# Performance work log

Measured on AMD Instinct MI355X. Metric: run time of the kernel, lower is better.

## Reference

```python
import jax, jax.numpy as jnp
import numpy as np

N = 1024    # num_points
HID = 1024  # Hamiltonian MLP hidden width


def setup_inputs() -> dict:
    key = jax.random.key(0)
    ks = jax.random.split(key, 6)
    def w(k, shape, fan_in):
        return jax.random.normal(k, shape, dtype=jnp.float32) / np.float32(np.sqrt(fan_in))
    return {
        "x": jax.random.normal(ks[0], (N,), dtype=jnp.float32),
        "q": jax.random.normal(ks[1], (N,), dtype=jnp.float32),
        "p": jax.random.normal(ks[2], (N,), dtype=jnp.float32),
        "W1": w(ks[3], (3 * N, HID), 3 * N),
        "b1": jnp.zeros((HID,), dtype=jnp.float32),
        "W2": w(ks[4], (HID, HID), HID),
        "b2": jnp.zeros((HID,), dtype=jnp.float32),
        "W3": w(ks[5], (HID, 1), HID),
        "b3": jnp.zeros((1,), dtype=jnp.float32),
    }


def _hamiltonian(z, W1, b1, W2, b2, W3, b3):
    # H: R^{3N} -> scalar (matches self.H(cat([x,q,p])).sum())
    h = jnp.tanh(z @ W1 + b1)
    h = jnp.tanh(h @ W2 + b2)
    return jnp.sum(h @ W3 + b3)


def reference(x, q, p, W1, b1, W2, b2, W3, b3):
    n = x.shape[0]

    def grads_qp(x_):
        # (dH/dq, dH/dp) as a function of x, with q,p closed over
        f = lambda q_, p_: _hamiltonian(jnp.concatenate([x_, q_, p_]), W1, b1, W2, b2, W3, b3)
        return jax.grad(f, argnums=(0, 1))(q, p)  # each [n]

    # Diagonal of cross-Hessian blocks via forward-over-reverse, batched over
    # all n basis directions at once (replaces the per-index autograd loop).
    eye = jnp.eye(n, dtype=x.dtype)

    def diag_entry(e_i, i):
        _, (dgq, dgp) = jax.jvp(grads_qp, (x,), (e_i,))
        return dgq[i], dgp[i]  # d2H/(dx_i dq_i), d2H/(dx_i dp_i)

    dH_dq_dx, dH_dp_dx = jax.vmap(diag_entry)(eye, jnp.arange(n))  # each [n]
    return dH_dp_dx, -dH_dq_dx
```

## Files before the change

kernel.cpp:

```cpp
#include <hip/hip_runtime.h>
#include <math.h>

typedef unsigned short u16;
typedef __bf16 bf16x8 __attribute__((ext_vector_type(8)));
typedef float f32x4 __attribute__((ext_vector_type(4)));

__device__ inline u16 bf16_rn(float x) {
    unsigned u = __float_as_uint(x);
    return (u16)((u + 0x7FFFu + ((u >> 16) & 1u)) >> 16);
}
__device__ inline void split2(float x, u16& h, u16& l) {
    h = bf16_rn(x);
    float hf = __uint_as_float(((unsigned)h) << 16);
    l = bf16_rn(x - hf);
}
__device__ inline uint2 pack4(u16 a, u16 b, u16 c, u16 d) {
    uint2 r;
    r.x = (unsigned)a | ((unsigned)b << 16);
    r.y = (unsigned)c | ((unsigned)d << 16);
    return r;
}
__device__ inline f32x4 mfma16(bf16x8 a, bf16x8 b, f32x4 c) {
    return __builtin_amdgcn_mfma_f32_16x16x32_bf16(a, b, c, 0, 0, 0);
}

__global__ __launch_bounds__(256) void k_init(const float* __restrict__ x,
                                              const float* __restrict__ q,
                                              const float* __restrict__ p,
                                              float* __restrict__ Z,
                                              float* __restrict__ out,
                                              float* __restrict__ uv) {
    int j = blockIdx.x * 256 + threadIdx.x;
    if (j < 2048) { out[j] = 0.f; uv[j] = 0.f; }
    Z[j] = (j < 1024) ? x[j] : (j < 2048 ? q[j - 1024] : p[j - 2048]);
}

__global__ __launch_bounds__(256) void k_u_partial(const float* __restrict__ W1,
                                                   const float* __restrict__ Z,
                                                   float* __restrict__ Uacc) {
    int k = blockIdx.x * 256 + threadIdx.x;
    int j0 = blockIdx.y * 64;
    __shared__ float zs[64];
    if (threadIdx.x < 64) zs[threadIdx.x] = Z[j0 + threadIdx.x];
    __syncthreads();
    float acc = 0.f;
#pragma unroll 8
    for (int j = 0; j < 64; ++j) acc += zs[j] * W1[(j0 + j) * 1024 + k];
    atomicAdd(&Uacc[k], acc);
}

__global__ __launch_bounds__(256) void k_h1(const float* __restrict__ Uacc,
                                            const float* __restrict__ b1,
                                            float* __restrict__ H1, float* __restrict__ D1) {
    int k = blockIdx.x * 256 + threadIdx.x;
    float h = tanhf(Uacc[k] + b1[k]);
    H1[k] = h;
    D1[k] = 1.f - h * h;
}

__global__ __launch_bounds__(256) void k_v_partial(const float* __restrict__ W2,
                                                   const float* __restrict__ H1,
                                                   float* __restrict__ Vacc) {
    int m = blockIdx.x * 256 + threadIdx.x;
    int k0 = blockIdx.y * 64;
    __shared__ float hs[64];
    if (threadIdx.x < 64) hs[threadIdx.x] = H1[k0 + threadIdx.x];
    __syncthreads();
    float acc = 0.f;
#pragma unroll 8
    for (int k = 0; k < 64; ++k) acc += hs[k] * W2[(k0 + k) * 1024 + m];
    atomicAdd(&Vacc[m], acc);
}

__global__ __launch_bounds__(256) void k_h2(const float* __restrict__ Vacc,
                                            const float* __restrict__ b2,
                                            const float* __restrict__ W3,
                                            float* __restrict__ Svec, float* __restrict__ Cvec) {
    int m = blockIdx.x * 256 + threadIdx.x;
    float h = tanhf(Vacc[m] + b2[m]);
    float d2 = 1.f - h * h;
    float w3 = W3[m];
    Svec[m] = d2 * w3;
    Cvec[m] = -2.f * h * d2 * w3;
}

__global__ __launch_bounds__(256) void k_g(const float* __restrict__ W2,
                                           const float* __restrict__ Svec,
                                           const float* __restrict__ H1,
                                           const float* __restrict__ D1,
                                           float* __restrict__ Avec) {
    int k = blockIdx.x;
    int t = threadIdx.x;
    float acc = 0.f;
#pragma unroll
    for (int m = t; m < 1024; m += 256) acc += W2[k * 1024 + m] * Svec[m];
    for (int o = 32; o; o >>= 1) acc += __shfl_down(acc, o);
    __shared__ float red[4];
    int lane = t & 63, w = t >> 6;
    if (lane == 0) red[w] = acc;
    __syncthreads();
    if (t == 0) Avec[k] = -2.f * H1[k] * D1[k] * (red[0] + red[1] + red[2] + red[3]);
}

__global__ __launch_bounds__(256) void k_prep_a(const float* __restrict__ W1,
                                                u16* __restrict__ Ah, u16* __restrict__ Al) {
    int idx = (blockIdx.x * 256 + threadIdx.x) * 4;
    float4 v = *(const float4*)(W1 + idx);
    u16 h0, l0, h1, l1, h2, l2, h3, l3;
    split2(v.x, h0, l0); split2(v.y, h1, l1); split2(v.z, h2, l2); split2(v.w, h3, l3);
    *(uint2*)&Ah[idx] = pack4(h0, h1, h2, h3);
    *(uint2*)&Al[idx] = pack4(l0, l1, l2, l3);
}

__global__ __launch_bounds__(256) void k_prep_w2(const float* __restrict__ W2,
                                                 const float* __restrict__ D1,
                                                 u16* __restrict__ W2h, u16* __restrict__ W2l,
                                                 u16* __restrict__ WTh, u16* __restrict__ WTl) {
    __shared__ float T[64][65];
    int k0 = blockIdx.y * 64, m0 = blockIdx.x * 64;
    int t = threadIdx.x;
    int rr = t >> 4, cc = (t & 15) * 4;
#pragma unroll
    for (int j = 0; j < 4; ++j) {
        int r = rr + j * 16;
        float4 v = *(const float4*)(W2 + (k0 + r) * 1024 + m0 + cc);
        T[r][cc + 0] = v.x; T[r][cc + 1] = v.y; T[r][cc + 2] = v.z; T[r][cc + 3] = v.w;
        u16 h0, l0, h1, l1, h2, l2, h3, l3;
        split2(v.x, h0, l0); split2(v.y, h1, l1); split2(v.z, h2, l2); split2(v.w, h3, l3);
        *(uint2*)&W2h[(k0 + r) * 1024 + m0 + cc] = pack4(h0, h1, h2, h3);
        *(uint2*)&W2l[(k0 + r) * 1024 + m0 + cc] = pack4(l0, l1, l2, l3);
    }
    __syncthreads();
#pragma unroll
    for (int j = 0; j < 4; ++j) {
        int mrow = rr + j * 16;
        float f0 = T[cc + 0][mrow] * D1[k0 + cc + 0];
        float f1 = T[cc + 1][mrow] * D1[k0 + cc + 1];
        float f2 = T[cc + 2][mrow] * D1[k0 + cc + 2];
        float f3 = T[cc + 3][mrow] * D1[k0 + cc + 3];
        u16 h0, l0, h1, l1, h2, l2, h3, l3;
        split2(f0, h0, l0); split2(f1, h1, l1); split2(f2, h2, l2); split2(f3, h3, l3);
        *(uint2*)&WTh[(m0 + mrow) * 1024 + k0 + cc] = pack4(h0, h1, h2, h3);
        *(uint2*)&WTl[(m0 + mrow) * 1024 + k0 + cc] = pack4(l0, l1, l2, l3);
    }
}

#define LDK 36
__global__ __launch_bounds__(256) void k_gemm1(const u16* __restrict__ Ah, const u16* __restrict__ Al,
                                               const u16* __restrict__ Bh, const u16* __restrict__ Bl,
                                               const float* __restrict__ Cvec,
                                               u16* __restrict__ Sh, u16* __restrict__ Sl) {
    __shared__ u16 As[2][2][64 * LDK];
    __shared__ u16 Bs[2][2][64 * LDK];
    int tid = threadIdx.x, lane = tid & 63, wv = tid >> 6;
    int wy = wv >> 1, wx = wv & 1;
    int i0 = blockIdx.y * 64, m0 = blockIdx.x * 64;
    int srow = tid >> 2, sseg = (tid & 3) * 8;
    int ldso = srow * LDK + sseg;
    const u16* ap_h = Ah + (i0 + srow) * 1024 + sseg;
    const u16* ap_l = Al + (i0 + srow) * 1024 + sseg;
    const u16* bp_h = Bh + (m0 + srow) * 1024 + sseg;
    const u16* bp_l = Bl + (m0 + srow) * 1024 + sseg;
    int tx = lane & 15, qy = lane >> 4;
    int ra0 = (wy * 32 + tx) * LDK + qy * 8;
    int ra1 = ra0 + 16 * LDK;
    int rb0 = (wx * 32 + tx) * LDK + qy * 8;
    int rb1 = rb0 + 16 * LDK;
    f32x4 acc[2][2];
#pragma unroll
    for (int a = 0; a < 2; ++a)
#pragma unroll
        for (int b = 0; b < 2; ++b) acc[a][b] = (f32x4){0.f, 0.f, 0.f, 0.f};

    {
        uint4 va_h = *(const uint4*)(ap_h);
        uint4 va_l = *(const uint4*)(ap_l);
        uint4 vb_h = *(const uint4*)(bp_h);
        uint4 vb_l = *(const uint4*)(bp_l);
        *(uint4*)&As[0][0][ldso] = va_h;
        *(uint4*)&As[0][1][ldso] = va_l;
        *(uint4*)&Bs[0][0][ldso] = vb_h;
        *(uint4*)&Bs[0][1][ldso] = vb_l;
    }

    for (int k0 = 0; k0 < 1024; k0 += 32) {
        int buf = (k0 >> 5) & 1;
        int kn = (k0 + 32) & 1023;
        uint4 na_h = *(const uint4*)(ap_h + kn);
        uint4 na_l = *(const uint4*)(ap_l + kn);
        uint4 nb_h = *(const uint4*)(bp_h + kn);
        uint4 nb_l = *(const uint4*)(bp_l + kn);
        __syncthreads();
        bf16x8 aH0 = *(const bf16x8*)&As[buf][0][ra0];
        bf16x8 aH1 = *(const bf16x8*)&As[buf][0][ra1];
        bf16x8 aL0 = *(const bf16x8*)&As[buf][1][ra0];
        bf16x8 aL1 = *(const bf16x8*)&As[buf][1][ra1];
        bf16x8 bH0 = *(const bf16x8*)&Bs[buf][0][rb0];
        bf16x8 bH1 = *(const bf16x8*)&Bs[buf][0][rb1];
        bf16x8 bL0 = *(const bf16x8*)&Bs[buf][1][rb0];
        bf16x8 bL1 = *(const bf16x8*)&Bs[buf][1][rb1];
        acc[0][0] = mfma16(aH0, bH0, acc[0][0]);
        acc[0][0] = mfma16(aH0, bL0, acc[0][0]);
        acc[0][0] = mfma16(aL0, bH0, acc[0][0]);
        acc[0][1] = mfma16(aH0, bH1, acc[0][1]);
        acc[0][1] = mfma16(aH0, bL1, acc[0][1]);
        acc[0][1] = mfma16(aL0, bH1, acc[0][1]);
        acc[1][0] = mfma16(aH1, bH0, acc[1][0]);
        acc[1][0] = mfma16(aH1, bL0, acc[1][0]);
        acc[1][0] = mfma16(aL1, bH0, acc[1][0]);
        acc[1][1] = mfma16(aH1, bH1, acc[1][1]);
        acc[1][1] = mfma16(aH1, bL1, acc[1][1]);
        acc[1][1] = mfma16(aL1, bH1, acc[1][1]);
        *(uint4*)&As[buf ^ 1][0][ldso] = na_h;
        *(uint4*)&As[buf ^ 1][1][ldso] = na_l;
        *(uint4*)&Bs[buf ^ 1][0][ldso] = nb_h;
        *(uint4*)&Bs[buf ^ 1][1][ldso] = nb_l;
    }
#pragma unroll
    for (int sj = 0; sj < 2; ++sj) {
        int m = m0 + wx * 32 + sj * 16 + tx;
        float cm = Cvec[m];
#pragma unroll
        for (int si = 0; si < 2; ++si) {
            int ib = i0 + wy * 32 + si * 16 + qy * 4;
#pragma unroll
            for (int r = 0; r < 4; ++r) {
                float v = acc[si][sj][r] * cm;
                u16 h, l;
                split2(v, h, l);
                Sh[(ib + r) * 1024 + m] = h;
                Sl[(ib + r) * 1024 + m] = l;
            }
        }
    }
}

__global__ __launch_bounds__(256) void k_gemm2(const u16* __restrict__ Sh, const u16* __restrict__ Sl,
                                               const u16* __restrict__ W2h, const u16* __restrict__ W2l,
                                               const float* __restrict__ W1,
                                               const float* __restrict__ D1,
                                               const float* __restrict__ Avec,
                                               float* __restrict__ out) {
    __shared__ u16 As[2][2][64 * LDK];
    __shared__ u16 Bs[2][2][64 * LDK];
    int tid = threadIdx.x, lane = tid & 63, wv = tid >> 6;
    int wy = wv >> 1, wx = wv & 1;
    int i0 = blockIdx.y * 64, k0g = blockIdx.x * 64;
    int srow = tid >> 2, sseg = (tid & 3) * 8;
    int ldso = srow * LDK + sseg;
    const u16* ap_h = Sh + (i0 + srow) * 1024 + sseg;
    const u16* ap_l = Sl + (i0 + srow) * 1024 + sseg;
    const u16* bp_h = W2h + (k0g + srow) * 1024 + sseg;
    const u16* bp_l = W2l + (k0g + srow) * 1024 + sseg;
    int tx = lane & 15, qy = lane >> 4;
    int ra0 = (wy * 32 + tx) * LDK + qy * 8;
    int ra1 = ra0 + 16 * LDK;
    int rb0 = (wx * 32 + tx) * LDK + qy * 8;
    int rb1 = rb0 + 16 * LDK;
    f32x4 acc[2][2];
#pragma unroll
    for (int a = 0; a < 2; ++a)
#pragma unroll
        for (int b = 0; b < 2; ++b) acc[a][b] = (f32x4){0.f, 0.f, 0.f, 0.f};

    {
        uint4 va_h = *(const uint4*)(ap_h);
        uint4 va_l = *(const uint4*)(ap_l);
        uint4 vb_h = *(const uint4*)(bp_h);
        uint4 vb_l = *(const uint4*)(bp_l);
        *(uint4*)&As[0][0][ldso] = va_h;
        *(uint4*)&As[0][1][ldso] = va_l;
        *(uint4*)&Bs[0][0][ldso] = vb_h;
        *(uint4*)&Bs[0][1][ldso] = vb_l;
    }

    for (int m0 = 0; m0 < 1024; m0 += 32) {
        int buf = (m0 >> 5) & 1;
        int mn = (m0 + 32) & 1023;
        uint4 na_h = *(const uint4*)(ap_h + mn);
        uint4 na_l = *(const uint4*)(ap_l + mn);
        uint4 nb_h = *(const uint4*)(bp_h + mn);
        uint4 nb_l = *(const uint4*)(bp_l + mn);
        __syncthreads();
        bf16x8 aH0 = *(const bf16x8*)&As[buf][0][ra0];
        bf16x8 aH1 = *(const bf16x8*)&As[buf][0][ra1];
        bf16x8 aL0 = *(const bf16x8*)&As[buf][1][ra0];
        bf16x8 aL1 = *(const bf16x8*)&As[buf][1][ra1];
        bf16x8 bH0 = *(const bf16x8*)&Bs[buf][0][rb0];
        bf16x8 bH1 = *(const bf16x8*)&Bs[buf][0][rb1];
        bf16x8 bL0 = *(const bf16x8*)&Bs[buf][1][rb0];
        bf16x8 bL1 = *(const bf16x8*)&Bs[buf][1][rb1];
        acc[0][0] = mfma16(aH0, bH0, acc[0][0]);
        acc[0][0] = mfma16(aH0, bL0, acc[0][0]);
        acc[0][0] = mfma16(aL0, bH0, acc[0][0]);
        acc[0][1] = mfma16(aH0, bH1, acc[0][1]);
        acc[0][1] = mfma16(aH0, bL1, acc[0][1]);
        acc[0][1] = mfma16(aL0, bH1, acc[0][1]);
        acc[1][0] = mfma16(aH1, bH0, acc[1][0]);
        acc[1][0] = mfma16(aH1, bL0, acc[1][0]);
        acc[1][0] = mfma16(aL1, bH0, acc[1][0]);
        acc[1][1] = mfma16(aH1, bH1, acc[1][1]);
        acc[1][1] = mfma16(aH1, bL1, acc[1][1]);
        acc[1][1] = mfma16(aL1, bH1, acc[1][1]);
        *(uint4*)&As[buf ^ 1][0][ldso] = na_h;
        *(uint4*)&As[buf ^ 1][1][ldso] = na_l;
        *(uint4*)&Bs[buf ^ 1][0][ldso] = nb_h;
        *(uint4*)&Bs[buf ^ 1][1][ldso] = nb_l;
    }
    int kk[2];
    float d1v[2], avv[2];
#pragma unroll
    for (int sj = 0; sj < 2; ++sj) {
        kk[sj] = k0g + wx * 32 + sj * 16 + tx;
        d1v[sj] = D1[kk[sj]];
        avv[sj] = Avec[kk[sj]];
    }
#pragma unroll
    for (int si = 0; si < 2; ++si) {
        int ib = i0 + wy * 32 + si * 16 + qy * 4;
#pragma unroll
        for (int r = 0; r < 4; ++r) {
            int i = ib + r;
            float pq = 0.f, pp = 0.f;
#pragma unroll
            for (int sj = 0; sj < 2; ++sj) {
                int k = kk[sj];
                float dr = avv[sj] * W1[i * 1024 + k] + d1v[sj] * acc[si][sj][r];
                pq += W1[(1024 + i) * 1024 + k] * dr;
                pp += W1[(2048 + i) * 1024 + k] * dr;
            }
            for (int o = 1; o < 16; o <<= 1) {
                pq += __shfl_xor(pq, o);
                pp += __shfl_xor(pp, o);
            }
            if (tx == 0) {
                atomicAdd(&out[i], pp);
                atomicAdd(&out[1024 + i], -pq);
            }
        }
    }
}

extern "C" void kernel_launch(void* const* d_in, const int* in_sizes, int n_in,
                              void* d_out, int out_size, void* d_ws, size_t ws_size,
                              hipStream_t stream) {
    const float* x = (const float*)d_in[0];
    const float* q = (const float*)d_in[1];
    const float* p = (const float*)d_in[2];
    const float* W1 = (const float*)d_in[3];
    const float* b1 = (const float*)d_in[4];
    const float* W2 = (const float*)d_in[5];
    const float* b2 = (const float*)d_in[6];
    const float* W3 = (const float*)d_in[7];
    float* out = (float*)d_out;
    float* ws = (float*)d_ws;
    float* H1 = ws, *D1 = ws + 1024, *Svec = ws + 2048, *Cvec = ws + 3072;
    float* Avec = ws + 4096, *Z = ws + 5120, *Uacc = ws + 8192;
    u16* u0 = (u16*)(ws + 16384);
    u16* Ah = u0;
    u16* Al = u0 + 1048576;
    u16* WTh = u0 + 2097152;
    u16* WTl = u0 + 3145728;
    u16* W2h = u0 + 4194304;
    u16* W2l = u0 + 5242880;
    u16* Sh = u0 + 6291456;
    u16* Sl = u0 + 7340032;

    k_init<<<12, 256, 0, stream>>>(x, q, p, Z, out, Uacc);
    k_prep_a<<<1024, 256, 0, stream>>>(W1, Ah, Al);
    k_u_partial<<<dim3(4, 48), 256, 0, stream>>>(W1, Z, Uacc);
    k_h1<<<4, 256, 0, stream>>>(Uacc, b1, H1, D1);
    k_prep_w2<<<dim3(16, 16), 256, 0, stream>>>(W2, D1, W2h, W2l, WTh, WTl);
    k_v_partial<<<dim3(4, 16), 256, 0, stream>>>(W2, H1, Uacc + 1024);
    k_h2<<<4, 256, 0, stream>>>(Uacc + 1024, b2, W3, Svec, Cvec);
    k_g<<<1024, 256, 0, stream>>>(W2, Svec, H1, D1, Avec);
    k_gemm1<<<dim3(16, 16), 256, 0, stream>>>(Ah, Al, WTh, WTl, Cvec, Sh, Sl);
    k_gemm2<<<dim3(16, 16), 256, 0, stream>>>(Sh, Sl, W2h, W2l, W1, D1, Avec, out);
}
```

Measured before the change: 137.5 us.

## Fuse pre-GEMM stages into fewer kernels and double GEMM K-tile depth

Merges init, W1 split, and the first matvec into one kernel that writes partials instead of using atomics. It folds the tanh of layer 1, the second matvec and the W2 split/transpose into a single pass over W2, and recomputes the layer-2 activation inside gemm1 and k_g. This cuts the launch count from ten to five. Both MFMA GEMMs now stage 64-wide K tiles, which halves the number of barriers. The cost is redundant tanh work in every block, more LDS per block, and 48-way partial sums read by each k_w2v block.

```diff
diff --git a/kernel.cpp b/kernel.cpp
--- a/kernel.cpp
+++ b/kernel.cpp
@@ -24,102 +24,66 @@
     return __builtin_amdgcn_mfma_f32_16x16x32_bf16(a, b, c, 0, 0, 0);
 }
 
-__global__ __launch_bounds__(256) void k_init(const float* __restrict__ x,
-                                              const float* __restrict__ q,
-                                              const float* __restrict__ p,
-                                              float* __restrict__ Z,
-                                              float* __restrict__ out,
-                                              float* __restrict__ uv) {
-    int j = blockIdx.x * 256 + threadIdx.x;
-    if (j < 2048) { out[j] = 0.f; uv[j] = 0.f; }
-    Z[j] = (j < 1024) ? x[j] : (j < 2048 ? q[j - 1024] : p[j - 2048]);
-}
-
-__global__ __launch_bounds__(256) void k_u_partial(const float* __restrict__ W1,
-                                                   const float* __restrict__ Z,
-                                                   float* __restrict__ Uacc) {
-    int k = blockIdx.x * 256 + threadIdx.x;
-    int j0 = blockIdx.y * 64;
-    __shared__ float zs[64];
-    if (threadIdx.x < 64) zs[threadIdx.x] = Z[j0 + threadIdx.x];
-    __syncthreads();
-    float acc = 0.f;
+__global__ __launch_bounds__(256) void k_pre(const float* __restrict__ x,
+                                             const float* __restrict__ q,
+                                             const float* __restrict__ p,
+                                             const float* __restrict__ W1,
+                                             u16* __restrict__ Ah, u16* __restrict__ Al,
+                                             float* __restrict__ Upart,
+                                             float* __restrict__ out,
+                                             float* __restrict__ Vacc) {
+    int b = blockIdx.x, t = threadIdx.x;
+    if (b < 1024) {
+        int idx = (b * 256 + t) * 4;
+        float4 v = *(const float4*)(W1 + idx);
+        u16 h0, l0, h1, l1, h2, l2, h3, l3;
+        split2(v.x, h0, l0); split2(v.y, h1, l1); split2(v.z, h2, l2); split2(v.w, h3, l3);
+        *(uint2*)&Ah[idx] = pack4(h0, h1, h2, h3);
+        *(uint2*)&Al[idx] = pack4(l0, l1, l2, l3);
+    } else if (b < 1216) {
+        int jc = b - 1024;
+        int k = (jc & 3) * 256 + t;
+        int j0 = (jc >> 2) * 64;
+        __shared__ float zs[64];
+        if (t < 64) {
+            int j = j0 + t;
+            zs[t] = (j < 1024) ? x[j] : (j < 2048 ? q[j - 1024] : p[j - 2048]);
+        }
+        __syncthreads();
+        float acc = 0.f;
 #pragma unroll 8
-    for (int j = 0; j < 64; ++j) acc += zs[j] * W1[(j0 + j) * 1024 + k];
-    atomicAdd(&Uacc[k], acc);
-}
-
-__global__ __launch_bounds__(256) void k_h1(const float* __restrict__ Uacc,
-                                            const float* __restrict__ b1,
-                                            float* __restrict__ H1, float* __restrict__ D1) {
-    int k = blockIdx.x * 256 + threadIdx.x;
-    float h = tanhf(Uacc[k] + b1[k]);
-    H1[k] = h;
-    D1[k] = 1.f - h * h;
-}
-
-__global__ __launch_bounds__(256) void k_v_partial(const float* __restrict__ W2,
-                                                   const float* __restrict__ H1,
-                                                   float* __restrict__ Vacc) {
-    int m = blockIdx.x * 256 + threadIdx.x;
-    int k0 = blockIdx.y * 64;
-    __shared__ float hs[64];
-    if (threadIdx.x < 64) hs[threadIdx.x] = H1[k0 + threadIdx.x];
-    __syncthreads();
-    float acc = 0.f;
-#pragma unroll 8
-    for (int k = 0; k < 64; ++k) acc += hs[k] * W2[(k0 + k) * 1024 + m];
-    atomicAdd(&Vacc[m], acc);
-}
-
-__global__ __launch_bounds__(256) void k_h2(const float* __restrict__ Vacc,
-                                            const float* __restrict__ b2,
-                                            const float* __restrict__ W3,
-                                            float* __restrict__ Svec, float* __restrict__ Cvec) {
-    int m = blockIdx.x * 256 + threadIdx.x;
-    float h = tanhf(Vacc[m] + b2[m]);
-    float d2 = 1.f - h * h;
-    float w3 = W3[m];
-    Svec[m] = d2 * w3;
-    Cvec[m] = -2.f * h * d2 * w3;
-}
-
-__global__ __launch_bounds__(256) void k_g(const float* __restrict__ W2,
-                                           const float* __restrict__ Svec,
-                                           const float* __restrict__ H1,
-                                           const float* __restrict__ D1,
-                                           float* __restrict__ Avec) {
-    int k = blockIdx.x;
-    int t = threadIdx.x;
-    float acc = 0.f;
-#pragma unroll
-    for (int m = t; m < 1024; m += 256) acc += W2[k * 1024 + m] * Svec[m];
-    for (int o = 32; o; o >>= 1) acc += __shfl_down(acc, o);
-    __shared__ float red[4];
-    int lane = t & 63, w = t >> 6;
-    if (lane == 0) red[w] = acc;
-    __syncthreads();
-    if (t == 0) Avec[k] = -2.f * H1[k] * D1[k] * (red[0] + red[1] + red[2] + red[3]);
-}
-
-__global__ __launch_bounds__(256) void k_prep_a(const float* __restrict__ W1,
-                                                u16* __restrict__ Ah, u16* __restrict__ Al) {
-    int idx = (blockIdx.x * 256 + threadIdx.x) * 4;
-    float4 v = *(const float4*)(W1 + idx);
-    u16 h0, l0, h1, l1, h2, l2, h3, l3;
-    split2(v.x, h0, l0); split2(v.y, h1, l1); split2(v.z, h2, l2); split2(v.w, h3, l3);
-    *(uint2*)&Ah[idx] = pack4(h0, h1, h2, h3);
-    *(uint2*)&Al[idx] = pack4(l0, l1, l2, l3);
-}
-
-__global__ __launch_bounds__(256) void k_prep_w2(const float* __restrict__ W2,
-                                                 const float* __restrict__ D1,
-                                                 u16* __restrict__ W2h, u16* __restrict__ W2l,
-                                                 u16* __restrict__ WTh, u16* __restrict__ WTl) {
+        for (int j = 0; j < 64; ++j) acc += zs[j] * W1[(j0 + j) * 1024 + k];
+        Upart[(jc >> 2) * 1024 + k] = acc;
+    } else {
+        int idx = ((b - 1216) * 256 + t) * 4;
+        if (idx < 2048) *(float4*)(out + idx) = make_float4(0.f, 0.f, 0.f, 0.f);
+        else *(float4*)(Vacc + idx - 2048) = make_float4(0.f, 0.f, 0.f, 0.f);
+    }
+}
+
+__global__ __launch_bounds__(256) void k_w2v(const float* __restrict__ W2,
+                                             const float* __restrict__ b1,
+                                             const float* __restrict__ Upart,
+                                             float* __restrict__ H1g, float* __restrict__ D1g,
+                                             u16* __restrict__ W2h, u16* __restrict__ W2l,
+                                             u16* __restrict__ WTh, u16* __restrict__ WTl,
+                                             float* __restrict__ Vacc) {
     __shared__ float T[64][65];
+    __shared__ float hs[64], ds[64];
     int k0 = blockIdx.y * 64, m0 = blockIdx.x * 64;
     int t = threadIdx.x;
+    if (t < 64) {
+        float u = 0.f;
+#pragma unroll 8
+        for (int c = 0; c < 48; ++c) u += Upart[c * 1024 + k0 + t];
+        float h = tanhf(u + b1[k0 + t]);
+        hs[t] = h;
+        ds[t] = 1.f - h * h;
+        if (m0 == 0) { H1g[k0 + t] = h; D1g[k0 + t] = 1.f - h * h; }
+    }
+    __syncthreads();
     int rr = t >> 4, cc = (t & 15) * 4;
+    float4 vp = make_float4(0.f, 0.f, 0.f, 0.f);
 #pragma unroll
     for (int j = 0; j < 4; ++j) {
         int r = rr + j * 16;
@@ -129,15 +93,27 @@
         split2(v.x, h0, l0); split2(v.y, h1, l1); split2(v.z, h2, l2); split2(v.w, h3, l3);
         *(uint2*)&W2h[(k0 + r) * 1024 + m0 + cc] = pack4(h0, h1, h2, h3);
         *(uint2*)&W2l[(k0 + r) * 1024 + m0 + cc] = pack4(l0, l1, l2, l3);
+        float hk = hs[r];
+        vp.x += hk * v.x; vp.y += hk * v.y; vp.z += hk * v.z; vp.w += hk * v.w;
+    }
+    vp.x += __shfl_xor(vp.x, 16); vp.y += __shfl_xor(vp.y, 16);
+    vp.z += __shfl_xor(vp.z, 16); vp.w += __shfl_xor(vp.w, 16);
+    vp.x += __shfl_xor(vp.x, 32); vp.y += __shfl_xor(vp.y, 32);
+    vp.z += __shfl_xor(vp.z, 32); vp.w += __shfl_xor(vp.w, 32);
+    if (((t & 63) >> 4) == 0) {
+        atomicAdd(&Vacc[m0 + cc + 0], vp.x);
+        atomicAdd(&Vacc[m0 + cc + 1], vp.y);
+        atomicAdd(&Vacc[m0 + cc + 2], vp.z);
+        atomicAdd(&Vacc[m0 + cc + 3], vp.w);
     }
     __syncthreads();
 #pragma unroll
     for (int j = 0; j < 4; ++j) {
         int mrow = rr + j * 16;
-        float f0 = T[cc + 0][mrow] * D1[k0 + cc + 0];
-        float f1 = T[cc + 1][mrow] * D1[k0 + cc + 1];
-        float f2 = T[cc + 2][mrow] * D1[k0 + cc + 2];
-        float f3 = T[cc + 3][mrow] * D1[k0 + cc + 3];
+        float f0 = T[cc + 0][mrow] * ds[cc + 0];
+        float f1 = T[cc + 1][mrow] * ds[cc + 1];
+        float f2 = T[cc + 2][mrow] * ds[cc + 2];
+        float f3 = T[cc + 3][mrow] * ds[cc + 3];
         u16 h0, l0, h1, l1, h2, l2, h3, l3;
         split2(f0, h0, l0); split2(f1, h1, l1); split2(f2, h2, l2); split2(f3, h3, l3);
         *(uint2*)&WTh[(m0 + mrow) * 1024 + k0 + cc] = pack4(h0, h1, h2, h3);
@@ -145,81 +121,114 @@
     }
 }
 
-#define LDK 36
+__global__ __launch_bounds__(256) void k_g(const float* __restrict__ W2,
+                                           const float* __restrict__ Vacc,
+                                           const float* __restrict__ b2,
+                                           const float* __restrict__ W3,
+                                           const float* __restrict__ H1,
+                                           const float* __restrict__ D1,
+                                           float* __restrict__ Avec) {
+    __shared__ float sv[1024];
+    int k = blockIdx.x;
+    int t = threadIdx.x;
+#pragma unroll
+    for (int j = 0; j < 4; ++j) {
+        int m = t * 4 + j;
+        float h = tanhf(Vacc[m] + b2[m]);
+        sv[m] = (1.f - h * h) * W3[m];
+    }
+    __syncthreads();
+    float acc = 0.f;
+#pragma unroll
+    for (int m = t; m < 1024; m += 256) acc += W2[k * 1024 + m] * sv[m];
+    for (int o = 32; o; o >>= 1) acc += __shfl_down(acc, o);
+    __shared__ float red[4];
+    int lane = t & 63, w = t >> 6;
+    if (lane == 0) red[w] = acc;
+    __syncthreads();
+    if (t == 0) Avec[k] = -2.f * H1[k] * D1[k] * (red[0] + red[1] + red[2] + red[3]);
+}
+
+#define LDK 68
 __global__ __launch_bounds__(256) void k_gemm1(const u16* __restrict__ Ah, const u16* __restrict__ Al,
                                                const u16* __restrict__ Bh, const u16* __restrict__ Bl,
-                                               const float* __restrict__ Cvec,
+                                               const float* __restrict__ Vacc,
+                                               const float* __restrict__ b2,
+                                               const float* __restrict__ W3,
                                                u16* __restrict__ Sh, u16* __restrict__ Sl) {
     __shared__ u16 As[2][2][64 * LDK];
     __shared__ u16 Bs[2][2][64 * LDK];
     int tid = threadIdx.x, lane = tid & 63, wv = tid >> 6;
     int wy = wv >> 1, wx = wv & 1;
     int i0 = blockIdx.y * 64, m0 = blockIdx.x * 64;
-    int srow = tid >> 2, sseg = (tid & 3) * 8;
+    int srow = tid >> 2, sseg = (tid & 3) * 16;
     int ldso = srow * LDK + sseg;
     const u16* ap_h = Ah + (i0 + srow) * 1024 + sseg;
     const u16* ap_l = Al + (i0 + srow) * 1024 + sseg;
     const u16* bp_h = Bh + (m0 + srow) * 1024 + sseg;
     const u16* bp_l = Bl + (m0 + srow) * 1024 + sseg;
     int tx = lane & 15, qy = lane >> 4;
-    int ra0 = (wy * 32 + tx) * LDK + qy * 8;
-    int ra1 = ra0 + 16 * LDK;
-    int rb0 = (wx * 32 + tx) * LDK + qy * 8;
-    int rb1 = rb0 + 16 * LDK;
+    int raA0 = (wy * 32 + tx) * LDK, raA1 = raA0 + 16 * LDK;
+    int rbB0 = (wx * 32 + tx) * LDK, rbB1 = rbB0 + 16 * LDK;
     f32x4 acc[2][2];
 #pragma unroll
     for (int a = 0; a < 2; ++a)
 #pragma unroll
         for (int b = 0; b < 2; ++b) acc[a][b] = (f32x4){0.f, 0.f, 0.f, 0.f};
 
-    {
-        uint4 va_h = *(const uint4*)(ap_h);
-        uint4 va_l = *(const uint4*)(ap_l);
-        uint4 vb_h = *(const uint4*)(bp_h);
-        uint4 vb_l = *(const uint4*)(bp_l);
-        *(uint4*)&As[0][0][ldso] = va_h;
-        *(uint4*)&As[0][1][ldso] = va_l;
-        *(uint4*)&Bs[0][0][ldso] = vb_h;
-        *(uint4*)&Bs[0][1][ldso] = vb_l;
-    }
-
-    for (int k0 = 0; k0 < 1024; k0 += 32) {
-        int buf = (k0 >> 5) & 1;
-        int kn = (k0 + 32) & 1023;
-        uint4 na_h = *(const uint4*)(ap_h + kn);
-        uint4 na_l = *(const uint4*)(ap_l + kn);
-        uint4 nb_h = *(const uint4*)(bp_h + kn);
-        uint4 nb_l = *(const uint4*)(bp_l + kn);
+    *(uint4*)&As[0][0][ldso] = *(const uint4*)(ap_h);
+    *(uint4*)&As[0][0][ldso + 8] = *(const uint4*)(ap_h + 8);
+    *(uint4*)&As[0][1][ldso] = *(const uint4*)(ap_l);
+    *(uint4*)&As[0][1][ldso + 8] = *(const uint4*)(ap_l + 8);
+    *(uint4*)&Bs[0][0][ldso] = *(const uint4*)(bp_h);
+    *(uint4*)&Bs[0][0][ldso + 8] = *(const uint4*)(bp_h + 8);
+    *(uint4*)&Bs[0][1][ldso] = *(const uint4*)(bp_l);
+    *(uint4*)&Bs[0][1][ldso + 8] = *(const uint4*)(bp_l + 8);
+
+    for (int k0 = 0; k0 < 1024; k0 += 64) {
+        int buf = (k0 >> 6) & 1;
+        int kn = (k0 + 64) & 1023;
+        uint4 pa0 = *(const uint4*)(ap_h + kn), pa1 = *(const uint4*)(ap_h + kn + 8);
+        uint4 pb0 = *(const uint4*)(ap_l + kn), pb1 = *(const uint4*)(ap_l + kn + 8);
+        uint4 pc0 = *(const uint4*)(bp_h + kn), pc1 = *(const uint4*)(bp_h + kn + 8);
+        uint4 pd0 = *(const uint4*)(bp_l + kn), pd1 = *(const uint4*)(bp_l + kn + 8);
         __syncthreads();
-        bf16x8 aH0 = *(const bf16x8*)&As[buf][0][ra0];
-        bf16x8 aH1 = *(const bf16x8*)&As[buf][0][ra1];
-        bf16x8 aL0 = *(const bf16x8*)&As[buf][1][ra0];
-        bf16x8 aL1 = *(const bf16x8*)&As[buf][1][ra1];
-        bf16x8 bH0 = *(const bf16x8*)&Bs[buf][0][rb0];
-        bf16x8 bH1 = *(const bf16x8*)&Bs[buf][0][rb1];
-        bf16x8 bL0 = *(const bf16x8*)&Bs[buf][1][rb0];
-        bf16x8 bL1 = *(const bf16x8*)&Bs[buf][1][rb1];
-        acc[0][0] = mfma16(aH0, bH0, acc[0][0]);
-        acc[0][0] = mfma16(aH0, bL0, acc[0][0]);
-        acc[0][0] = mfma16(aL0, bH0, acc[0][0]);
-        acc[0][1] = mfma16(aH0, bH1, acc[0][1]);
-        acc[0][1] = mfma16(aH0, bL1, acc[0][1]);
-        acc[0][1] = mfma16(aL0, bH1, acc[0][1]);
-        acc[1][0] = mfma16(aH1, bH0, acc[1][0]);
-        acc[1][0] = mfma16(aH1, bL0, acc[1][0]);
-        acc[1][0] = mfma16(aL1, bH0, acc[1][0]);
-        acc[1][1] = mfma16(aH1, bH1, acc[1][1]);
-        acc[1][1] = mfma16(aH1, bL1, acc[1][1]);
-        acc[1][1] = mfma16(aL1, bH1, acc[1][1]);
-        *(uint4*)&As[buf ^ 1][0][ldso] = na_h;
-        *(uint4*)&As[buf ^ 1][1][ldso] = na_l;
-        *(uint4*)&Bs[buf ^ 1][0][ldso] = nb_h;
-        *(uint4*)&Bs[buf ^ 1][1][ldso] = nb_l;
+#pragma unroll
+        for (int ks = 0; ks < 2; ++ks) {
+            int o = ks * 32 + qy * 8;
+            bf16x8 aH0 = *(const bf16x8*)&As[buf][0][raA0 + o];
+            bf16x8 aH1 = *(const bf16x8*)&As[buf][0][raA1 + o];
+            bf16x8 aL0 = *(const bf16x8*)&As[buf][1][raA0 + o];
+            bf16x8 aL1 = *(const bf16x8*)&As[buf][1][raA1 + o];
+            bf16x8 bH0 = *(const bf16x8*)&Bs[buf][0][rbB0 + o];
+            bf16x8 bH1 = *(const bf16x8*)&Bs[buf][0][rbB1 + o];
+            bf16x8 bL0 = *(const bf16x8*)&Bs[buf][1][rbB0 + o];
+            bf16x8 bL1 = *(const bf16x8*)&Bs[buf][1][rbB1 + o];
+            acc[0][0] = mfma16(aH0, bH0, acc[0][0]);
+            acc[0][0] = mfma16(aH0, bL0, acc[0][0]);
+            acc[0][0] = mfma16(aL0, bH0, acc[0][0]);
+            acc[0][1] = mfma16(aH0, bH1, acc[0][1]);
+            acc[0][1] = mfma16(aH0, bL1, acc[0][1]);
+            acc[0][1] = mfma16(aL0, bH1, acc[0][1]);
+            acc[1][0] = mfma16(aH1, bH0, acc[1][0]);
+            acc[1][0] = mfma16(aH1, bL0, acc[1][0]);
+            acc[1][0] = mfma16(aL1, bH0, acc[1][0]);
+            acc[1][1] = mfma16(aH1, bH1, acc[1][1]);
+            acc[1][1] = mfma16(aH1, bL1, acc[1][1]);
+            acc[1][1] = mfma16(aL1, bH1, acc[1][1]);
+        }
+        int nb = buf ^ 1;
+        *(uint4*)&As[nb][0][ldso] = pa0; *(uint4*)&As[nb][0][ldso + 8] = pa1;
+        *(uint4*)&As[nb][1][ldso] = pb0; *(uint4*)&As[nb][1][ldso + 8] = pb1;
+        *(uint4*)&Bs[nb][0][ldso] = pc0; *(uint4*)&Bs[nb][0][ldso + 8] = pc1;
+        *(uint4*)&Bs[nb][1][ldso] = pd0; *(uint4*)&Bs[nb][1][ldso + 8] = pd1;
     }
 #pragma unroll
     for (int sj = 0; sj < 2; ++sj) {
         int m = m0 + wx * 32 + sj * 16 + tx;
-        float cm = Cvec[m];
+        float hv = tanhf(Vacc[m] + b2[m]);
+        float d2 = 1.f - hv * hv;
+        float cm = -2.f * hv * d2 * W3[m];
 #pragma unroll
         for (int si = 0; si < 2; ++si) {
             int ib = i0 + wy * 32 + si * 16 + qy * 4;
@@ -246,66 +255,67 @@
     int tid = threadIdx.x, lane = tid & 63, wv = tid >> 6;
     int wy = wv >> 1, wx = wv & 1;
     int i0 = blockIdx.y * 64, k0g = blockIdx.x * 64;
-    int srow = tid >> 2, sseg = (tid & 3) * 8;
+    int srow = tid >> 2, sseg = (tid & 3) * 16;
     int ldso = srow * LDK + sseg;
     const u16* ap_h = Sh + (i0 + srow) * 1024 + sseg;
     const u16* ap_l = Sl + (i0 + srow) * 1024 + sseg;
     const u16* bp_h = W2h + (k0g + srow) * 1024 + sseg;
     const u16* bp_l = W2l + (k0g + srow) * 1024 + sseg;
     int tx = lane & 15, qy = lane >> 4;
-    int ra0 = (wy * 32 + tx) * LDK + qy * 8;
-    int ra1 = ra0 + 16 * LDK;
-    int rb0 = (wx * 32 + tx) * LDK + qy * 8;
-    int rb1 = rb0 + 16 * LDK;
+    int raA0 = (wy * 32 + tx) * LDK, raA1 = raA0 + 16 * LDK;
+    int rbB0 = (wx * 32 + tx) * LDK, rbB1 = rbB0 + 16 * LDK;
     f32x4 acc[2][2];
 #pragma unroll
     for (int a = 0; a < 2; ++a)
 #pragma unroll
         for (int b = 0; b < 2; ++b) acc[a][b] = (f32x4){0.f, 0.f, 0.f, 0.f};
 
-    {
-        uint4 va_h = *(const uint4*)(ap_h);
-        uint4 va_l = *(const uint4*)(ap_l);
-        uint4 vb_h = *(const uint4*)(bp_h);
-        uint4 vb_l = *(const uint4*)(bp_l);
-        *(uint4*)&As[0][0][ldso] = va_h;
-        *(uint4*)&As[0][1][ldso] = va_l;
-        *(uint4*)&Bs[0][0][ldso] = vb_h;
-        *(uint4*)&Bs[0][1][ldso] = vb_l;
-    }
-
-    for (int m0 = 0; m0 < 1024; m0 += 32) {
-        int buf = (m0 >> 5) & 1;
-        int mn = (m0 + 32) & 1023;
-        uint4 na_h = *(const uint4*)(ap_h + mn);
-        uint4 na_l = *(const uint4*)(ap_l + mn);
-        uint4 nb_h = *(const uint4*)(bp_h + mn);
-        uint4 nb_l = *(const uint4*)(bp_l + mn);
+    *(uint4*)&As[0][0][ldso] = *(const uint4*)(ap_h);
+    *(uint4*)&As[0][0][ldso + 8] = *(const uint4*)(ap_h + 8);
+    *(uint4*)&As[0][1][ldso] = *(const uint4*)(ap_l);
+    *(uint4*)&As[0][1][ldso + 8] = *(const uint4*)(ap_l + 8);
+    *(uint4*)&Bs[0][0][ldso] = *(const uint4*)(bp_h);
+    *(uint4*)&Bs[0][0][ldso + 8] = *(const uint4*)(bp_h + 8);
+    *(uint4*)&Bs[0][1][ldso] = *(const uint4*)(bp_l);
+    *(uint4*)&Bs[0][1][ldso + 8] = *(const uint4*)(bp_l + 8);
+
+    for (int m0 = 0; m0 < 1024; m0 += 64) {
+        int buf = (m0 >> 6) & 1;
+        int mn = (m0 + 64) & 1023;
+        uint4 pa0 = *(const uint4*)(ap_h + mn), pa1 = *(const uint4*)(ap_h + mn + 8);
+        uint4 pb0 = *(const uint4*)(ap_l + mn), pb1 = *(const uint4*)(ap_l + mn + 8);
+        uint4 pc0 = *(const uint4*)(bp_h + mn), pc1 = *(const uint4*)(bp_h + mn + 8);
+        uint4 pd0 = *(const uint4*)(bp_l + mn), pd1 = *(const uint4*)(bp_l + mn + 8);
         __syncthreads();
-        bf16x8 aH0 = *(const bf16x8*)&As[buf][0][ra0];
-        bf16x8 aH1 = *(const bf16x8*)&As[buf][0][ra1];
-        bf16x8 aL0 = *(const bf16x8*)&As[buf][1][ra0];
-        bf16x8 aL1 = *(const bf16x8*)&As[buf][1][ra1];
-        bf16x8 bH0 = *(const bf16x8*)&Bs[buf][0][rb0];
-        bf16x8 bH1 = *(const bf16x8*)&Bs[buf][0][rb1];
-        bf16x8 bL0 = *(const bf16x8*)&Bs[buf][1][rb0];
-        bf16x8 bL1 = *(const bf16x8*)&Bs[buf][1][rb1];
-        acc[0][0] = mfma16(aH0, bH0, acc[0][0]);
-        acc[0][0] = mfma16(aH0, bL0, acc[0][0]);
-        acc[0][0] = mfma16(aL0, bH0, acc[0][0]);
-        acc[0][1] = mfma16(aH0, bH1, acc[0][1]);
-        acc[0][1] = mfma16(aH0, bL1, acc[0][1]);
-        acc[0][1] = mfma16(aL0, bH1, acc[0][1]);
-        acc[1][0] = mfma16(aH1, bH0, acc[1][0]);
-        acc[1][0] = mfma16(aH1, bL0, acc[1][0]);
-        acc[1][0] = mfma16(aL1, bH0, acc[1][0]);
-        acc[1][1] = mfma16(aH1, bH1, acc[1][1]);
-        acc[1][1] = mfma16(aH1, bL1, acc[1][1]);
-        acc[1][1] = mfma16(aL1, bH1, acc[1][1]);
-        *(uint4*)&As[buf ^ 1][0][ldso] = na_h;
-        *(uint4*)&As[buf ^ 1][1][ldso] = na_l;
-        *(uint4*)&Bs[buf ^ 1][0][ldso] = nb_h;
-        *(uint4*)&Bs[buf ^ 1][1][ldso] = nb_l;
+#pragma unroll
+        for (int ks = 0; ks < 2; ++ks) {
+            int o = ks * 32 + qy * 8;
+            bf16x8 aH0 = *(const bf16x8*)&As[buf][0][raA0 + o];
+            bf16x8 aH1 = *(const bf16x8*)&As[buf][0][raA1 + o];
+            bf16x8 aL0 = *(const bf16x8*)&As[buf][1][raA0 + o];
+            bf16x8 aL1 = *(const bf16x8*)&As[buf][1][raA1 + o];
+            bf16x8 bH0 = *(const bf16x8*)&Bs[buf][0][rbB0 + o];
+            bf16x8 bH1 = *(const bf16x8*)&Bs[buf][0][rbB1 + o];
+            bf16x8 bL0 = *(const bf16x8*)&Bs[buf][1][rbB0 + o];
+            bf16x8 bL1 = *(const bf16x8*)&Bs[buf][1][rbB1 + o];
+            acc[0][0] = mfma16(aH0, bH0, acc[0][0]);
+            acc[0][0] = mfma16(aH0, bL0, acc[0][0]);
+            acc[0][0] = mfma16(aL0, bH0, acc[0][0]);
+            acc[0][1] = mfma16(aH0, bH1, acc[0][1]);
+            acc[0][1] = mfma16(aH0, bL1, acc[0][1]);
+            acc[0][1] = mfma16(aL0, bH1, acc[0][1]);
+            acc[1][0] = mfma16(aH1, bH0, acc[1][0]);
+            acc[1][0] = mfma16(aH1, bL0, acc[1][0]);
+            acc[1][0] = mfma16(aL1, bH0, acc[1][0]);
+            acc[1][1] = mfma16(aH1, bH1, acc[1][1]);
+            acc[1][1] = mfma16(aH1, bL1, acc[1][1]);
+            acc[1][1] = mfma16(aL1, bH1, acc[1][1]);
+        }
+        int nb = buf ^ 1;
+        *(uint4*)&As[nb][0][ldso] = pa0; *(uint4*)&As[nb][0][ldso + 8] = pa1;
+        *(uint4*)&As[nb][1][ldso] = pb0; *(uint4*)&As[nb][1][ldso + 8] = pb1;
+        *(uint4*)&Bs[nb][0][ldso] = pc0; *(uint4*)&Bs[nb][0][ldso + 8] = pc1;
+        *(uint4*)&Bs[nb][1][ldso] = pd0; *(uint4*)&Bs[nb][1][ldso + 8] = pd1;
     }
     int kk[2];
     float d1v[2], avv[2];
@@ -354,9 +364,9 @@
     const float* W3 = (const float*)d_in[7];
     float* out = (float*)d_out;
     float* ws = (float*)d_ws;
-    float* H1 = ws, *D1 = ws + 1024, *Svec = ws + 2048, *Cvec = ws + 3072;
-    float* Avec = ws + 4096, *Z = ws + 5120, *Uacc = ws + 8192;
-    u16* u0 = (u16*)(ws + 16384);
+    float* H1 = ws, *D1 = ws + 1024, *Avec = ws + 2048, *Vacc = ws + 3072;
+    float* Upart = ws + 4096;
+    u16* u0 = (u16*)(ws + 65536);
     u16* Ah = u0;
     u16* Al = u0 + 1048576;
     u16* WTh = u0 + 2097152;
@@ -366,14 +376,9 @@
     u16* Sh = u0 + 6291456;
     u16* Sl = u0 + 7340032;
 
-    k_init<<<12, 256, 0, stream>>>(x, q, p, Z, out, Uacc);
-    k_prep_a<<<1024, 256, 0, stream>>>(W1, Ah, Al);
-    k_u_partial<<<dim3(4, 48), 256, 0, stream>>>(W1, Z, Uacc);
-    k_h1<<<4, 256, 0, stream>>>(Uacc, b1, H1, D1);
-    k_prep_w2<<<dim3(16, 16), 256, 0, stream>>>(W2, D1, W2h, W2l, WTh, WTl);
-    k_v_partial<<<dim3(4, 16), 256, 0, stream>>>(W2, H1, Uacc + 1024);
-    k_h2<<<4, 256, 0, stream>>>(Uacc + 1024, b2, W3, Svec, Cvec);
-    k_g<<<1024, 256, 0, stream>>>(W2, Svec, H1, D1, Avec);
-    k_gemm1<<<dim3(16, 16), 256, 0, stream>>>(Ah, Al, WTh, WTl, Cvec, Sh, Sl);
+    k_pre<<<1219, 256, 0, stream>>>(x, q, p, W1, Ah, Al, Upart, out, Vacc);
+    k_w2v<<<dim3(16, 16), 256, 0, stream>>>(W2, b1, Upart, H1, D1, W2h, W2l, WTh, WTl, Vacc);
+    k_gemm1<<<dim3(16, 16), 256, 0, stream>>>(Ah, Al, WTh, WTl, Vacc, b2, W3, Sh, Sl);
+    k_g<<<1024, 256, 0, stream>>>(W2, Vacc, b2, W3, H1, D1, Avec);
     k_gemm2<<<dim3(16, 16), 256, 0, stream>>>(Sh, Sl, W2h, W2l, W1, D1, Avec, out);
 }
```

Result: faster. 131.5 us (-4.3%).
